# Optimization experiments

Hardware: AMD Instinct MI355X
Metric: run time of the kernel (lower is better)

Reference implementation:

```python
import jax, jax.numpy as jnp
import numpy as np

B, N, D = 8, 1024, 768
R, SH = 10, 2
H = R + SH            # 12 total heads
DH = D // H           # 64
DF = 2 * D            # FFN hidden


def _layernorm(x, g, b, eps=1e-5):
    mu = jnp.mean(x, axis=-1, keepdims=True)
    var = jnp.var(x, axis=-1, keepdims=True)
    return (x - mu) * jax.lax.rsqrt(var + eps) * g + b


def setup_inputs() -> dict:
    key = jax.random.key(0)
    ks = jax.random.split(key, 12)
    s = 0.02
    inp = {
        'nodes': jax.random.normal(ks[0], (B, N, D), dtype=jnp.float32),
        'relation_mask': jax.random.uniform(ks[1], (B, N, N, R), dtype=jnp.float32),
        'node_mask': jax.random.randint(ks[2], (B, N), 0, 2).astype(bool),
        'Wq': jax.random.normal(ks[3], (D, D), dtype=jnp.float32) * s,
        'bq': jnp.zeros((D,), jnp.float32),
        'Wk': jax.random.normal(ks[4], (D, D), dtype=jnp.float32) * s,
        'bk': jnp.zeros((D,), jnp.float32),
        'Wv': jax.random.normal(ks[5], (D, D), dtype=jnp.float32) * s,
        'bv': jnp.zeros((D,), jnp.float32),
        'Wo': jax.random.normal(ks[6], (D, D), dtype=jnp.float32) * s,
        'bo': jnp.zeros((D,), jnp.float32),
        'ln1_g': jnp.ones((D,), jnp.float32),
        'ln1_b': jnp.zeros((D,), jnp.float32),
        'W1': jax.random.normal(ks[7], (DF, D), dtype=jnp.float32) * s,
        'b1': jnp.zeros((DF,), jnp.float32),
        'W2': jax.random.normal(ks[8], (D, DF), dtype=jnp.float32) * s,
        'b2': jnp.zeros((D,), jnp.float32),
        'ln2_g': jnp.ones((D,), jnp.float32),
        'ln2_b': jnp.zeros((D,), jnp.float32),
    }
    return inp


def reference(nodes, relation_mask, node_mask, Wq, bq, Wk, bk, Wv, bv, Wo, bo,
              ln1_g, ln1_b, W1, b1, W2, b2, ln2_g, ln2_b):
    neg_inf = jnp.float32(-jnp.inf)
    # projections -> [B, H, N, DH]
    q = (nodes @ Wq.T + bq).reshape(B, N, H, DH).transpose(0, 2, 1, 3)
    k = (nodes @ Wk.T + bk).reshape(B, N, H, DH).transpose(0, 2, 1, 3)
    v = (nodes @ Wv.T + bv).reshape(B, N, H, DH).transpose(0, 2, 1, 3)
    scores = jnp.einsum('bhqd,bhkd->bhqk', q, k) / jnp.sqrt(jnp.float32(DH))
    # relation-typed gating on first R heads
    rel_gate = relation_mask.transpose(0, 3, 1, 2)          # [B, R, N, N]
    typed = jnp.where(rel_gate < 1e-4, neg_inf, scores[:, :R])
    scores = jnp.concatenate([typed, scores[:, R:]], axis=1)
    # key padding mask
    key_mask = node_mask[:, None, None, :]                  # [B,1,1,N]
    scores = jnp.where(key_mask, scores, neg_inf)
    attn = jax.nn.softmax(scores, axis=-1)
    attn = jnp.nan_to_num(attn, nan=0.0)                    # rows with no valid keys -> 0
    out = jnp.einsum('bhqk,bhkd->bhqd', attn, v)
    out = out.transpose(0, 2, 1, 3).reshape(B, N, D)
    out = out @ Wo.T + bo
    h = _layernorm(nodes + out, ln1_g, ln1_b)
    ffn = jax.nn.gelu(h @ W1.T + b1, approximate=False) @ W2.T + b2
    h = _layernorm(h + ffn, ln2_g, ln2_b)
    return h
```

## Files before the change

### kernel.cpp

```cpp
#include <hip/hip_runtime.h>
#include <stdint.h>
#include <math.h>

typedef unsigned short u16;
typedef __bf16 bf16x8 __attribute__((ext_vector_type(8)));
typedef __bf16 bf16x2 __attribute__((ext_vector_type(2)));
typedef unsigned short u16x8 __attribute__((ext_vector_type(8)));
typedef float f32x4 __attribute__((ext_vector_type(4)));

#define DEVI __device__ __forceinline__

constexpr int B_ = 8, N_ = 1024, D_ = 768, H_ = 12, DH_ = 64, DF_ = 1536;

DEVI u16 f2bu(float f) {
  unsigned x = __builtin_bit_cast(unsigned, f);
  x += 0x7FFFu + ((x >> 16) & 1u);
  return (u16)(x >> 16);
}
DEVI float b2f(u16 u) { return __builtin_bit_cast(float, (unsigned)u << 16); }

DEVI bf16x8 ld_frag(const u16* p) {
  return __builtin_bit_cast(bf16x8, *(const u16x8*)p);
}

DEVI void gload_lds16(const u16* g, u16* l) {
  __builtin_amdgcn_global_load_lds(
      (const __attribute__((address_space(1))) void*)g,
      (__attribute__((address_space(3))) void*)l, 16, 0, 0);
}

struct CvtArgs {
  const float* src[7];
  u16* dst[7];
  int n4[7];
  int start[8];
};
__global__ __launch_bounds__(256)
void prep_all(CvtArgs a, const float* __restrict__ rel, const int* __restrict__ nm,
              u16* __restrict__ mp) {
  const int gb0 = blockIdx.x;
  const int t = threadIdx.x;
  if (gb0 < 2048) {
    const int b = gb0 >> 8, q0 = ((gb0 >> 2) & 63) * 16, k0 = (gb0 & 3) * 256;
    __shared__ u16 w12[16][256];
    const int key_ok = nm[(b << 10) + k0 + t];
    const float th = 1e-4f;
#pragma unroll 1
    for (int it = 0; it < 16; ++it) {
      unsigned bits;
      if (!key_ok) {
        bits = 0xFFFu;
      } else {
        const size_t idx = (((size_t)(b << 10) + q0 + it) << 10) + k0 + t;
        const float2* rp = (const float2*)(rel + idx * 10);
        float2 a0 = rp[0], a1 = rp[1], a2 = rp[2], a3 = rp[3], a4 = rp[4];
        bits  = (a0.x < th ? 1u : 0u)   | (a0.y < th ? 2u : 0u)
              | (a1.x < th ? 4u : 0u)   | (a1.y < th ? 8u : 0u)
              | (a2.x < th ? 16u : 0u)  | (a2.y < th ? 32u : 0u)
              | (a3.x < th ? 64u : 0u)  | (a3.y < th ? 128u : 0u)
              | (a4.x < th ? 256u : 0u) | (a4.y < th ? 512u : 0u);
      }
      w12[it][t ^ ((it & 7) << 1)] = (u16)bits;
    }
    __syncthreads();
    const int ql = t & 15, kt = t >> 4;
    unsigned wv[16];
#pragma unroll
    for (int j2 = 0; j2 < 8; ++j2) {
      const int e = (kt * 16 + j2 * 2) ^ ((ql & 7) << 1);
      wv[j2 * 2] = w12[ql][e];
      wv[j2 * 2 + 1] = w12[ql][e + 1];
    }
#pragma unroll
    for (int h = 0; h < 12; ++h) {
      unsigned word = 0;
#pragma unroll
      for (int j = 0; j < 16; ++j) word |= ((wv[j] >> h) & 1u) << j;
      mp[(((size_t)(b * H_ + h)) * (N_ / 16) + (k0 >> 4) + kt) * N_ + q0 + ql] = (u16)word;
    }
  } else {
    int j = 0;
    while (gb0 >= a.start[j + 1]) ++j;
    const int i = (gb0 - a.start[j]) * 256 + t;
    if (i >= a.n4[j]) return;
    float4 v = ((const float4*)a.src[j])[i];
    ushort4 o;
    o.x = f2bu(v.x); o.y = f2bu(v.y); o.z = f2bu(v.z); o.w = f2bu(v.w);
    ((ushort4*)a.dst[j])[i] = o;
  }
}

template<int EPI>
DEVI void gemm_body(const u16* __restrict__ A, const u16* __restrict__ Bm,
                    const float* __restrict__ bias0, const float* __restrict__ bias1,
                    const float* __restrict__ residf, const u16* __restrict__ residb,
                    u16* __restrict__ out0, u16* __restrict__ out1,
                    int N, int K, int bx, int by,
                    u16 (&As)[3][128 * 32], u16 (&Bs)[3][128 * 32]) {
  const int t = threadIdx.x;
  const int w = t >> 6, l = t & 63;
  const int li = l & 15, grp = l >> 4;
  const int n0 = bx * 128, m0 = by * 128;
  const int wr = w >> 1, wc = w & 1;

  f32x4 acc[4][4] = {};

  const int arow = w * 16 + (l >> 2);
  const int acol = (l & 3) * 8;
  const u16* Ag = A + (size_t)(m0 + arow) * K + acol;
  const u16* Bg = Bm + (size_t)(n0 + arow) * K + acol;
  const int NT = K >> 5;

  auto stage = [&](int buf, int kt) {
    u16* Asw = &As[buf][(w * 16) * 32];
    u16* Bsw = &Bs[buf][(w * 16) * 32];
    const int k0 = kt * 32;
    gload_lds16(Ag + k0, Asw);
    gload_lds16(Ag + (size_t)64 * K + k0, Asw + 64 * 32);
    gload_lds16(Bg + k0, Bsw);
    gload_lds16(Bg + (size_t)64 * K + k0, Bsw + 64 * 32);
  };

  stage(0, 0); stage(1, 1);
  asm volatile("s_waitcnt vmcnt(4)\n\ts_barrier" ::: "memory");

  for (int kt = 0; kt < NT; ++kt) {
    const int bt = kt % 3;
    const bool pre = (kt + 2 < NT);
    if (pre) stage((kt + 2) % 3, kt + 2);
    bf16x8 af[4], bfr[4];
#pragma unroll
    for (int m = 0; m < 4; ++m)
      af[m] = ld_frag(&As[bt][(wr * 64 + m * 16 + li) * 32 + grp * 8]);
#pragma unroll
    for (int n = 0; n < 4; ++n)
      bfr[n] = ld_frag(&Bs[bt][(wc * 64 + n * 16 + li) * 32 + grp * 8]);
    __builtin_amdgcn_s_setprio(1);
#pragma unroll
    for (int m = 0; m < 4; ++m)
#pragma unroll
      for (int n = 0; n < 4; ++n)
        acc[m][n] = __builtin_amdgcn_mfma_f32_16x16x32_bf16(af[m], bfr[n], acc[m][n], 0, 0, 0);
    __builtin_amdgcn_s_setprio(0);
    if (pre) asm volatile("s_waitcnt vmcnt(4) lgkmcnt(0)\n\ts_barrier" ::: "memory");
    else     asm volatile("s_waitcnt vmcnt(0) lgkmcnt(0)\n\ts_barrier" ::: "memory");
  }

#pragma unroll
  for (int m = 0; m < 4; ++m) {
#pragma unroll
    for (int n = 0; n < 4; ++n) {
#pragma unroll
      for (int j = 0; j < 4; ++j) {
        const int row = m0 + wr * 64 + m * 16 + grp * 4 + j;
        const int col = n0 + wc * 64 + n * 16 + li;
        float v = acc[m][n][j];
        if constexpr (EPI == 0) {
          v += (col < D_) ? bias0[col] : bias1[col - D_];
          if (col < D_) v *= 0.125f;
          const int b = row >> 10, i = row & (N_ - 1);
          int c2 = (col < D_) ? col : col - D_;
          u16* dst = (col < D_) ? out0 : out1;
          dst[(((size_t)(b * H_ + (c2 >> 6))) * N_ + i) * DH_ + (c2 & 63)] = f2bu(v);
        } else if constexpr (EPI == 1) {
          v += bias0[row];
          const int b = col >> 10, i = col & (N_ - 1);
          out0[(((size_t)(b * H_ + (row >> 6))) * DH_ + (row & 63)) * N_ + i] = f2bu(v);
        } else if constexpr (EPI == 2) {
          v += bias0[col] + residf[(size_t)row * N + col];
          out0[(size_t)row * N + col] = f2bu(v);
        } else if constexpr (EPI == 3) {
          v += bias0[col];
          float gel = 0.5f * v * (1.0f + erff(v * 0.70710678118654752440f));
          out0[(size_t)row * N + col] = f2bu(gel);
        } else {
          v += bias0[col] + b2f(residb[(size_t)row * N + col]);
          out0[(size_t)row * N + col] = f2bu(v);
        }
      }
    }
  }
}

template<int EPI>
__global__ __launch_bounds__(256, 3)
void gemm_bt(const u16* __restrict__ A, const u16* __restrict__ Bm,
             const float* __restrict__ bias0,
             const float* __restrict__ residf, const u16* __restrict__ residb,
             u16* __restrict__ out0, int N, int K) {
  __shared__ u16 As[3][128 * 32];
  __shared__ u16 Bs[3][128 * 32];
  const int nwg = gridDim.x * gridDim.y;
  int id = blockIdx.y * gridDim.x + blockIdx.x;
  id = (id & 7) * (nwg >> 3) + (id >> 3);
  const int by = id / gridDim.x;
  const int bx = id - by * gridDim.x;
  gemm_body<EPI>(A, Bm, bias0, nullptr, residf, residb, out0, nullptr,
                 N, K, bx, by, As, Bs);
}

__global__ __launch_bounds__(256, 3)
void gemm_qkv(const u16* __restrict__ Xbf, const u16* __restrict__ Wqk,
              const u16* __restrict__ Wv,
              const float* __restrict__ bq, const float* __restrict__ bk,
              const float* __restrict__ bv,
              u16* __restrict__ qb, u16* __restrict__ kb, u16* __restrict__ vTb) {
  __shared__ u16 As[3][128 * 32];
  __shared__ u16 Bs[3][128 * 32];
  constexpr int nwg = 1152;
  int id = blockIdx.x;
  id = (id & 7) * (nwg >> 3) + (id >> 3);
  if (id < 768) {
    const int by = id / 12, bx = id - by * 12;
    gemm_body<0>(Xbf, Wqk, bq, bk, nullptr, nullptr, qb, kb,
                 1536, 768, bx, by, As, Bs);
  } else {
    const int v = id - 768;
    const int by = v / 64, bx = v - by * 64;
    gemm_body<1>(Wv, Xbf, bv, nullptr, nullptr, nullptr, vTb, nullptr,
                 8192, 768, bx, by, As, Bs);
  }
}

__global__ __launch_bounds__(512, 4)
void attn(const u16* __restrict__ q, const u16* __restrict__ k, const u16* __restrict__ vT,
          const u16* __restrict__ mp, u16* __restrict__ outp) {
  const int nwg = gridDim.x;
  const int p = blockIdx.x;
  const int lid = (p & 7) * (nwg >> 3) + (p >> 3);
  const int bh_i = lid >> 3;
  const int qblk = lid & 7;
  const int b = bh_i / H_, h = bh_i - (bh_i / H_) * H_;
  const int w = threadIdx.x >> 6, l = threadIdx.x & 63;
  const int li = l & 15, grp = l >> 4;
  const int qw = qblk * 128 + w * 16;
  const size_t bh = (size_t)bh_i;

  __shared__ u16 Kt[2][64 * 64];
  __shared__ u16 Vt[2][64 * 64];
  __shared__ u16 P[8][16 * 64];

  const u16* kbase = k + bh * N_ * DH_;
  const u16* vbase = vT + bh * DH_ * N_;

  const int srow_off = l >> 3;
  const int sg = l & 7;
  const int r0 = w * 8;
  auto stageK = [&](int buf, int kj0) {
    const int row = r0 + srow_off;
    const int gp = sg ^ (row & 7);
    gload_lds16(kbase + (size_t)(kj0 + row) * DH_ + gp * 8, &Kt[buf][r0 * 64]);
  };
  auto stageV = [&](int buf, int kj0) {
    const int row = r0 + srow_off;
    const int gp = sg ^ (row & 7);
    gload_lds16(vbase + (size_t)row * N_ + kj0 + gp * 8, &Vt[buf][r0 * 64]);
  };

  const u16* qp = q + (bh * N_ + qw) * DH_;
  const bf16x8 bq0 = ld_frag(qp + li * DH_ + grp * 8);
  const bf16x8 bq1 = ld_frag(qp + li * DH_ + 32 + grp * 8);

  f32x4 accO[4] = {};
  float m = -INFINITY, lsum = 0.f;

  u16* Pw = &P[w][0];
  const int sw = (li & 7) << 3;
  const int prow = li * 64;
  const u16* mrow = mp + bh * (N_ / 16) * N_ + qw + li;

  stageK(0, 0); stageV(0, 0);
  __syncthreads();
  int cur = 0;

  for (int kj0 = 0; kj0 < N_; kj0 += 64) {
    if (kj0 + 64 < N_) { stageK(cur ^ 1, kj0 + 64); stageV(cur ^ 1, kj0 + 64); }
    unsigned mword[4];
#pragma unroll
    for (int t = 0; t < 4; ++t) mword[t] = mrow[(size_t)((kj0 >> 4) + t) * N_];

    f32x4 s[4];
    __builtin_amdgcn_s_setprio(1);
#pragma unroll
    for (int t = 0; t < 4; ++t) {
      const int row = t * 16 + li;
      const int rs = row & 7;
      const bf16x8 ka0 = ld_frag(&Kt[cur][row * 64 + ((grp ^ rs) * 8)]);
      const bf16x8 ka1 = ld_frag(&Kt[cur][row * 64 + (((grp + 4) ^ rs) * 8)]);
      f32x4 z = {0.f, 0.f, 0.f, 0.f};
      z = __builtin_amdgcn_mfma_f32_16x16x32_bf16(ka0, bq0, z, 0, 0, 0);
      z = __builtin_amdgcn_mfma_f32_16x16x32_bf16(ka1, bq1, z, 0, 0, 0);
      s[t] = z;
    }
    __builtin_amdgcn_s_setprio(0);

    float sv[16];
#pragma unroll
    for (int t = 0; t < 4; ++t) {
      const unsigned mb = (mword[t] >> (grp * 4)) & 0xFu;
#pragma unroll
      for (int j = 0; j < 4; ++j)
        sv[t * 4 + j] = ((mb >> j) & 1u) ? -INFINITY : s[t][j];
    }
    const float a0 = fmaxf(fmaxf(sv[0], sv[1]), sv[2]);
    const float a1 = fmaxf(fmaxf(sv[3], sv[4]), sv[5]);
    const float a2 = fmaxf(fmaxf(sv[6], sv[7]), sv[8]);
    const float a3 = fmaxf(fmaxf(sv[9], sv[10]), sv[11]);
    const float a4 = fmaxf(fmaxf(sv[12], sv[13]), sv[14]);
    float rmax = fmaxf(fmaxf(fmaxf(a0, a1), fmaxf(a2, a3)), fmaxf(a4, sv[15]));
    rmax = fmaxf(rmax, __shfl_xor(rmax, 16));
    rmax = fmaxf(rmax, __shfl_xor(rmax, 32));
    if (!__all(rmax <= m + 8.f)) {
      const float mnew = fmaxf(m, rmax);
      const float scal = (m == -INFINITY) ? 0.f : __expf(m - mnew);
      lsum *= scal;
#pragma unroll
      for (int t2 = 0; t2 < 4; ++t2) accO[t2] *= scal;
      m = mnew;
    }
    const float msafe = (m == -INFINITY) ? 0.f : m;
    float psum = 0.f;
    float pv[16];
#pragma unroll
    for (int i = 0; i < 16; ++i) {
      const float e = __expf(sv[i] - msafe);
      pv[i] = e;
      psum += e;
    }
    psum += __shfl_xor(psum, 16);
    psum += __shfl_xor(psum, 32);
    lsum += psum;
#pragma unroll
    for (int t = 0; t < 4; ++t) {
      bf16x2 plo = { (__bf16)pv[t * 4 + 0], (__bf16)pv[t * 4 + 1] };
      bf16x2 phi = { (__bf16)pv[t * 4 + 2], (__bf16)pv[t * 4 + 3] };
      uint2 pk;
      pk.x = __builtin_bit_cast(unsigned, plo);
      pk.y = __builtin_bit_cast(unsigned, phi);
      *(uint2*)&Pw[prow + ((t * 16 + grp * 4) ^ sw)] = pk;
    }
    __builtin_amdgcn_s_setprio(1);
#pragma unroll
    for (int kc = 0; kc < 2; ++kc) {
      const bf16x8 pb = ld_frag(&Pw[prow + ((kc * 32 + grp * 8) ^ sw)]);
#pragma unroll
      for (int t2 = 0; t2 < 4; ++t2) {
        const int row = t2 * 16 + li;
        const bf16x8 va = ld_frag(&Vt[cur][row * 64 + (((kc * 4 + grp) ^ (row & 7)) * 8)]);
        accO[t2] = __builtin_amdgcn_mfma_f32_16x16x32_bf16(va, pb, accO[t2], 0, 0, 0);
      }
    }
    __builtin_amdgcn_s_setprio(0);
    __syncthreads();
    cur ^= 1;
  }
  const float inv = (lsum > 0.f) ? 1.0f / lsum : 0.f;
  u16* op = outp + ((size_t)b * N_ + qw + li) * D_ + h * DH_;
#pragma unroll
  for (int t2 = 0; t2 < 4; ++t2) {
    bf16x2 o01 = { (__bf16)(accO[t2][0] * inv), (__bf16)(accO[t2][1] * inv) };
    bf16x2 o23 = { (__bf16)(accO[t2][2] * inv), (__bf16)(accO[t2][3] * inv) };
    uint2 ov;
    ov.x = __builtin_bit_cast(unsigned, o01);
    ov.y = __builtin_bit_cast(unsigned, o23);
    *(uint2*)&op[t2 * 16 + grp * 4] = ov;
  }
}

template<int OUTF32>
__global__ __launch_bounds__(256)
void ln_kernel(const u16* __restrict__ x, const float* __restrict__ g,
               const float* __restrict__ be, u16* __restrict__ ybf,
               float* __restrict__ yf) {
  const int row = blockIdx.x;
  const int t = threadIdx.x;
  const u16* xr = x + (size_t)row * D_;
  const float v0 = b2f(xr[t]), v1 = b2f(xr[t + 256]), v2 = b2f(xr[t + 512]);
  float s = v0 + v1 + v2;
  float s2 = v0 * v0 + v1 * v1 + v2 * v2;
#pragma unroll
  for (int d = 1; d < 64; d <<= 1) { s += __shfl_xor(s, d); s2 += __shfl_xor(s2, d); }
  __shared__ float red[8];
  const int w = t >> 6;
  if ((t & 63) == 0) { red[w] = s; red[4 + w] = s2; }
  __syncthreads();
  s = red[0] + red[1] + red[2] + red[3];
  s2 = red[4] + red[5] + red[6] + red[7];
  const float mu = s * (1.0f / D_);
  const float var = fmaxf(s2 * (1.0f / D_) - mu * mu, 0.0f);
  const float rstd = rsqrtf(var + 1e-5f);
#pragma unroll
  for (int c = 0; c < 3; ++c) {
    const int idx = t + c * 256;
    const float vv = (c == 0) ? v0 : (c == 1) ? v1 : v2;
    const float o = (vv - mu) * rstd * g[idx] + be[idx];
    if constexpr (OUTF32) yf[(size_t)row * D_ + idx] = o;
    else ybf[(size_t)row * D_ + idx] = f2bu(o);
  }
}

extern "C" void kernel_launch(void* const* d_in, const int* in_sizes, int n_in,
                              void* d_out, int out_size, void* d_ws, size_t ws_size,
                              hipStream_t stream) {
  (void)in_sizes; (void)n_in; (void)out_size; (void)ws_size;
  const float* nodes = (const float*)d_in[0];
  const float* rel   = (const float*)d_in[1];
  const int*   nmask = (const int*)d_in[2];
  const float* Wq = (const float*)d_in[3];
  const float* bq = (const float*)d_in[4];
  const float* Wk = (const float*)d_in[5];
  const float* bk = (const float*)d_in[6];
  const float* Wv = (const float*)d_in[7];
  const float* bv = (const float*)d_in[8];
  const float* Wo = (const float*)d_in[9];
  const float* bo = (const float*)d_in[10];
  const float* ln1g = (const float*)d_in[11];
  const float* ln1b = (const float*)d_in[12];
  const float* W1 = (const float*)d_in[13];
  const float* b1 = (const float*)d_in[14];
  const float* W2 = (const float*)d_in[15];
  const float* b2 = (const float*)d_in[16];
  const float* ln2g = (const float*)d_in[17];
  const float* ln2b = (const float*)d_in[18];
  float* out = (float*)d_out;

  char* ws = (char*)d_ws;
  u16* Wqk_bf = (u16*)(ws + 0);
  u16* Wv_bf  = (u16*)(ws + 2359296);
  u16* Wo_bf  = (u16*)(ws + 3538944);
  u16* W1_bf  = (u16*)(ws + 4718592);
  u16* W2_bf  = (u16*)(ws + 7077888);
  u16* Xbf    = (u16*)(ws + 9437184);
  u16* qb     = (u16*)(ws + 22020096);
  u16* kb     = (u16*)(ws + 34603008);
  u16* vTb    = (u16*)(ws + 47185920);
  u16* mwb    = (u16*)(ws + 59768832);
  u16* prehb  = (u16*)(ws + 22020096);
  u16* hbf    = (u16*)(ws + 47185920);
  u16* f1b    = (u16*)(ws + 59768832);
  u16* preob  = (u16*)(ws + 84934656);
  u16* attno  = Xbf;

  const dim3 blk(256);
  CvtArgs ca;
  ca.src[0] = Wq; ca.src[1] = Wk; ca.src[2] = Wv; ca.src[3] = Wo;
  ca.src[4] = W1; ca.src[5] = W2; ca.src[6] = nodes;
  ca.dst[0] = Wqk_bf; ca.dst[1] = Wqk_bf + 768 * 768; ca.dst[2] = Wv_bf;
  ca.dst[3] = Wo_bf; ca.dst[4] = W1_bf; ca.dst[5] = W2_bf; ca.dst[6] = Xbf;
  ca.n4[0] = ca.n4[1] = ca.n4[2] = ca.n4[3] = 147456;
  ca.n4[4] = ca.n4[5] = 294912; ca.n4[6] = 1572864;
  ca.start[0] = 2048; ca.start[1] = 2624; ca.start[2] = 3200; ca.start[3] = 3776;
  ca.start[4] = 4352; ca.start[5] = 5504; ca.start[6] = 6656; ca.start[7] = 12800;
  prep_all<<<12800, blk, 0, stream>>>(ca, rel, nmask, mwb);
  gemm_qkv<<<1152, blk, 0, stream>>>(Xbf, Wqk_bf, Wv_bf, bq, bk, bv, qb, kb, vTb);
  attn<<<768, dim3(512), 0, stream>>>(qb, kb, vTb, mwb, attno);
  gemm_bt<2><<<dim3(6, 64), blk, 0, stream>>>(attno, Wo_bf, bo, nodes, nullptr,
                                              prehb, 768, 768);
  ln_kernel<0><<<8192, blk, 0, stream>>>(prehb, ln1g, ln1b, hbf, nullptr);
  gemm_bt<3><<<dim3(12, 64), blk, 0, stream>>>(hbf, W1_bf, b1, nullptr, nullptr,
                                               f1b, 1536, 768);
  gemm_bt<4><<<dim3(6, 64), blk, 0, stream>>>(f1b, W2_bf, b2, nullptr, hbf,
                                              preob, 768, 1536);
  ln_kernel<1><<<8192, blk, 0, stream>>>(preob, ln2g, ln2b, nullptr, out);
}
```

Baseline: 298.5 us.

## Fuse relation-mask packing into QKV GEMM kernel to overlap bandwidth and compute

The relation-mask bit-packing work, which streams the large fp32 relation tensor, moves out of the conversion kernel and into the QKV GEMM launch. Blocks are interleaved in groups of 16 mask blocks and 9 GEMM tiles, so the memory-bound mask work runs alongside the matrix-core GEMM. The mask blocks reuse the GEMM's LDS buffer as scratch. The cost is that mask blocks now carry the GEMM kernel's LDS allocation and launch bounds, which can lower their occupancy, and the tile swizzle is recomputed.

Result: slower. 312.0 us (+4.5%).

```diff
diff --git a/kernel.cpp b/kernel.cpp
--- a/kernel.cpp
+++ b/kernel.cpp
@@ -36,58 +36,16 @@
   int start[8];
 };
 __global__ __launch_bounds__(256)
-void prep_all(CvtArgs a, const float* __restrict__ rel, const int* __restrict__ nm,
-              u16* __restrict__ mp) {
-  const int gb0 = blockIdx.x;
-  const int t = threadIdx.x;
-  if (gb0 < 2048) {
-    const int b = gb0 >> 8, q0 = ((gb0 >> 2) & 63) * 16, k0 = (gb0 & 3) * 256;
-    __shared__ u16 w12[16][256];
-    const int key_ok = nm[(b << 10) + k0 + t];
-    const float th = 1e-4f;
-#pragma unroll 1
-    for (int it = 0; it < 16; ++it) {
-      unsigned bits;
-      if (!key_ok) {
-        bits = 0xFFFu;
-      } else {
-        const size_t idx = (((size_t)(b << 10) + q0 + it) << 10) + k0 + t;
-        const float2* rp = (const float2*)(rel + idx * 10);
-        float2 a0 = rp[0], a1 = rp[1], a2 = rp[2], a3 = rp[3], a4 = rp[4];
-        bits  = (a0.x < th ? 1u : 0u)   | (a0.y < th ? 2u : 0u)
-              | (a1.x < th ? 4u : 0u)   | (a1.y < th ? 8u : 0u)
-              | (a2.x < th ? 16u : 0u)  | (a2.y < th ? 32u : 0u)
-              | (a3.x < th ? 64u : 0u)  | (a3.y < th ? 128u : 0u)
-              | (a4.x < th ? 256u : 0u) | (a4.y < th ? 512u : 0u);
-      }
-      w12[it][t ^ ((it & 7) << 1)] = (u16)bits;
-    }
-    __syncthreads();
-    const int ql = t & 15, kt = t >> 4;
-    unsigned wv[16];
-#pragma unroll
-    for (int j2 = 0; j2 < 8; ++j2) {
-      const int e = (kt * 16 + j2 * 2) ^ ((ql & 7) << 1);
-      wv[j2 * 2] = w12[ql][e];
-      wv[j2 * 2 + 1] = w12[ql][e + 1];
-    }
-#pragma unroll
-    for (int h = 0; h < 12; ++h) {
-      unsigned word = 0;
-#pragma unroll
-      for (int j = 0; j < 16; ++j) word |= ((wv[j] >> h) & 1u) << j;
-      mp[(((size_t)(b * H_ + h)) * (N_ / 16) + (k0 >> 4) + kt) * N_ + q0 + ql] = (u16)word;
-    }
-  } else {
-    int j = 0;
-    while (gb0 >= a.start[j + 1]) ++j;
-    const int i = (gb0 - a.start[j]) * 256 + t;
-    if (i >= a.n4[j]) return;
-    float4 v = ((const float4*)a.src[j])[i];
-    ushort4 o;
-    o.x = f2bu(v.x); o.y = f2bu(v.y); o.z = f2bu(v.z); o.w = f2bu(v.w);
-    ((ushort4*)a.dst[j])[i] = o;
-  }
+void cvt_all(CvtArgs a) {
+  const int gb = blockIdx.x;
+  int j = 0;
+  while (gb >= a.start[j + 1]) ++j;
+  const int i = (gb - a.start[j]) * 256 + threadIdx.x;
+  if (i >= a.n4[j]) return;
+  float4 v = ((const float4*)a.src[j])[i];
+  ushort4 o;
+  o.x = f2bu(v.x); o.y = f2bu(v.y); o.z = f2bu(v.z); o.w = f2bu(v.w);
+  ((ushort4*)a.dst[j])[i] = o;
 }
 
 template<int EPI>
@@ -200,25 +158,70 @@
 }
 
 __global__ __launch_bounds__(256, 3)
-void gemm_qkv(const u16* __restrict__ Xbf, const u16* __restrict__ Wqk,
+void mask_qkv(const float* __restrict__ rel, const int* __restrict__ nm,
+              u16* __restrict__ mp,
+              const u16* __restrict__ Xbf, const u16* __restrict__ Wqk,
               const u16* __restrict__ Wv,
               const float* __restrict__ bq, const float* __restrict__ bk,
               const float* __restrict__ bv,
               u16* __restrict__ qb, u16* __restrict__ kb, u16* __restrict__ vTb) {
   __shared__ u16 As[3][128 * 32];
   __shared__ u16 Bs[3][128 * 32];
-  constexpr int nwg = 1152;
-  int id = blockIdx.x;
-  id = (id & 7) * (nwg >> 3) + (id >> 3);
-  if (id < 768) {
-    const int by = id / 12, bx = id - by * 12;
-    gemm_body<0>(Xbf, Wqk, bq, bk, nullptr, nullptr, qb, kb,
-                 1536, 768, bx, by, As, Bs);
+  const int id0 = blockIdx.x;
+  const int g = id0 / 25, r = id0 - g * 25;
+  const int t = threadIdx.x;
+  if (r < 16) {
+    const int mb = g * 16 + r;
+    const int b = mb >> 8, q0 = ((mb >> 2) & 63) * 16, k0 = (mb & 3) * 256;
+    u16 (*w12)[256] = (u16(*)[256])&As[0][0];
+    const int key_ok = nm[(b << 10) + k0 + t];
+    const float th = 1e-4f;
+#pragma unroll 1
+    for (int it = 0; it < 16; ++it) {
+      unsigned bits;
+      if (!key_ok) {
+        bits = 0xFFFu;
+      } else {
+        const size_t idx = (((size_t)(b << 10) + q0 + it) << 10) + k0 + t;
+        const float2* rp = (const float2*)(rel + idx * 10);
+        float2 a0 = rp[0], a1 = rp[1], a2 = rp[2], a3 = rp[3], a4 = rp[4];
+        bits  = (a0.x < th ? 1u : 0u)   | (a0.y < th ? 2u : 0u)
+              | (a1.x < th ? 4u : 0u)   | (a1.y < th ? 8u : 0u)
+              | (a2.x < th ? 16u : 0u)  | (a2.y < th ? 32u : 0u)
+              | (a3.x < th ? 64u : 0u)  | (a3.y < th ? 128u : 0u)
+              | (a4.x < th ? 256u : 0u) | (a4.y < th ? 512u : 0u);
+      }
+      w12[it][t ^ ((it & 7) << 1)] = (u16)bits;
+    }
+    __syncthreads();
+    const int ql = t & 15, kt = t >> 4;
+    unsigned wv[16];
+#pragma unroll
+    for (int j2 = 0; j2 < 8; ++j2) {
+      const int e = (kt * 16 + j2 * 2) ^ ((ql & 7) << 1);
+      wv[j2 * 2] = w12[ql][e];
+      wv[j2 * 2 + 1] = w12[ql][e + 1];
+    }
+#pragma unroll
+    for (int h = 0; h < 12; ++h) {
+      unsigned word = 0;
+#pragma unroll
+      for (int j = 0; j < 16; ++j) word |= ((wv[j] >> h) & 1u) << j;
+      mp[(((size_t)(b * H_ + h)) * (N_ / 16) + (k0 >> 4) + kt) * N_ + q0 + ql] = (u16)word;
+    }
   } else {
-    const int v = id - 768;
-    const int by = v / 64, bx = v - by * 64;
-    gemm_body<1>(Wv, Xbf, bv, nullptr, nullptr, nullptr, vTb, nullptr,
-                 8192, 768, bx, by, As, Bs);
+    int gid = g * 9 + (r - 16);
+    gid = (gid & 7) * 144 + (gid >> 3);
+    if (gid < 768) {
+      const int by = gid / 12, bx = gid - by * 12;
+      gemm_body<0>(Xbf, Wqk, bq, bk, nullptr, nullptr, qb, kb,
+                   1536, 768, bx, by, As, Bs);
+    } else {
+      const int v = gid - 768;
+      const int by = v / 64, bx = v - by * 64;
+      gemm_body<1>(Wv, Xbf, bv, nullptr, nullptr, nullptr, vTb, nullptr,
+                   8192, 768, bx, by, As, Bs);
+    }
   }
 }
 
@@ -449,10 +452,11 @@
   ca.dst[3] = Wo_bf; ca.dst[4] = W1_bf; ca.dst[5] = W2_bf; ca.dst[6] = Xbf;
   ca.n4[0] = ca.n4[1] = ca.n4[2] = ca.n4[3] = 147456;
   ca.n4[4] = ca.n4[5] = 294912; ca.n4[6] = 1572864;
-  ca.start[0] = 2048; ca.start[1] = 2624; ca.start[2] = 3200; ca.start[3] = 3776;
-  ca.start[4] = 4352; ca.start[5] = 5504; ca.start[6] = 6656; ca.start[7] = 12800;
-  prep_all<<<12800, blk, 0, stream>>>(ca, rel, nmask, mwb);
-  gemm_qkv<<<1152, blk, 0, stream>>>(Xbf, Wqk_bf, Wv_bf, bq, bk, bv, qb, kb, vTb);
+  ca.start[0] = 0; ca.start[1] = 576; ca.start[2] = 1152; ca.start[3] = 1728;
+  ca.start[4] = 2304; ca.start[5] = 3456; ca.start[6] = 4608; ca.start[7] = 10752;
+  cvt_all<<<10752, blk, 0, stream>>>(ca);
+  mask_qkv<<<3200, blk, 0, stream>>>(rel, nmask, mwb, Xbf, Wqk_bf, Wv_bf,
+                                     bq, bk, bv, qb, kb, vTb);
   attn<<<768, dim3(512), 0, stream>>>(qb, kb, vTb, mwb, attno);
   gemm_bt<2><<<dim3(6, 64), blk, 0, stream>>>(attno, Wo_bf, bo, nodes, nullptr,
                                               prehb, 768, 768);
```

## Compact valid keys per batch and skip masked keys in mask, V, and attention

Applied to the files above, without the earlier changes.

A new compaction kernel builds, per batch, a list of valid key indices and a padded count. Mask building, the V projection and the attention loop then run only over those compacted keys, skipping padded-out keys; K is gathered through the index list and V^T is written in compacted order. Separately, the Q scale absorbs log2(e) so the softmax uses exp2f with an adjusted rescale threshold. This adds an extra launch and gather indirection, and the speedup depends on the fraction of masked keys (about half with random masks).

After: 312.3 us. +4.6%, slower.

```diff
diff --git a/kernel.cpp b/kernel.cpp
--- a/kernel.cpp
+++ b/kernel.cpp
@@ -11,6 +11,8 @@
 #define DEVI __device__ __forceinline__
 
 constexpr int B_ = 8, N_ = 1024, D_ = 768, H_ = 12, DH_ = 64, DF_ = 1536;
+constexpr float QSCALE = 0.18033688011112042f;
+constexpr float THR2 = 11.5415603f;
 
 DEVI u16 f2bu(float f) {
   unsigned x = __builtin_bit_cast(unsigned, f);
@@ -27,6 +29,28 @@
   __builtin_amdgcn_global_load_lds(
       (const __attribute__((address_space(1))) void*)g,
       (__attribute__((address_space(3))) void*)l, 16, 0, 0);
+}
+
+__global__ __launch_bounds__(1024)
+void compact(const int* __restrict__ nm, int* __restrict__ idx,
+             int* __restrict__ nkparr) {
+  const int b = blockIdx.x, t = threadIdx.x;
+  const int wave = t >> 6, lane = t & 63;
+  const bool valid = nm[b * N_ + t] != 0;
+  const unsigned long long ball = __ballot(valid);
+  const int pre = (int)__popcll(ball & ((1ull << lane) - 1ull));
+  __shared__ int wsum[16];
+  if (lane == 0) wsum[wave] = (int)__popcll(ball);
+  __syncthreads();
+  int base = 0;
+#pragma unroll
+  for (int i = 0; i < 16; ++i) base += (i < wave) ? wsum[i] : 0;
+  int total = 0;
+#pragma unroll
+  for (int i = 0; i < 16; ++i) total += wsum[i];
+  if (valid) idx[b * N_ + base + pre] = t;
+  if (t < N_ - total) idx[b * N_ + total + t] = 0;
+  if (t == 0) { nkparr[b] = (total + 63) & ~63; nkparr[8 + b] = total; }
 }
 
 struct CvtArgs {
@@ -36,23 +60,28 @@
   int start[8];
 };
 __global__ __launch_bounds__(256)
-void prep_all(CvtArgs a, const float* __restrict__ rel, const int* __restrict__ nm,
+void prep_all(CvtArgs a, const float* __restrict__ rel,
+              const int* __restrict__ idx, const int* __restrict__ nkparr,
               u16* __restrict__ mp) {
   const int gb0 = blockIdx.x;
   const int t = threadIdx.x;
   if (gb0 < 2048) {
     const int b = gb0 >> 8, q0 = ((gb0 >> 2) & 63) * 16, k0 = (gb0 & 3) * 256;
+    const int nkp = nkparr[b], nk = nkparr[8 + b];
+    if (k0 >= nkp) return;
+    const int s = k0 + t;
+    const int tok = idx[b * N_ + s];
+    const bool vs = (s < nk);
     __shared__ u16 w12[16][256];
-    const int key_ok = nm[(b << 10) + k0 + t];
     const float th = 1e-4f;
 #pragma unroll 1
     for (int it = 0; it < 16; ++it) {
       unsigned bits;
-      if (!key_ok) {
+      if (!vs) {
         bits = 0xFFFu;
       } else {
-        const size_t idx = (((size_t)(b << 10) + q0 + it) << 10) + k0 + t;
-        const float2* rp = (const float2*)(rel + idx * 10);
+        const size_t ridx = (((size_t)(b << 10) + q0 + it) << 10) + tok;
+        const float2* rp = (const float2*)(rel + ridx * 10);
         float2 a0 = rp[0], a1 = rp[1], a2 = rp[2], a3 = rp[3], a4 = rp[4];
         bits  = (a0.x < th ? 1u : 0u)   | (a0.y < th ? 2u : 0u)
               | (a1.x < th ? 4u : 0u)   | (a1.y < th ? 8u : 0u)
@@ -157,15 +186,11 @@
         float v = acc[m][n][j];
         if constexpr (EPI == 0) {
           v += (col < D_) ? bias0[col] : bias1[col - D_];
-          if (col < D_) v *= 0.125f;
+          if (col < D_) v *= QSCALE;
           const int b = row >> 10, i = row & (N_ - 1);
           int c2 = (col < D_) ? col : col - D_;
           u16* dst = (col < D_) ? out0 : out1;
           dst[(((size_t)(b * H_ + (c2 >> 6))) * N_ + i) * DH_ + (c2 & 63)] = f2bu(v);
-        } else if constexpr (EPI == 1) {
-          v += bias0[row];
-          const int b = col >> 10, i = col & (N_ - 1);
-          out0[(((size_t)(b * H_ + (row >> 6))) * DH_ + (row & 63)) * N_ + i] = f2bu(v);
         } else if constexpr (EPI == 2) {
           v += bias0[col] + residf[(size_t)row * N + col];
           out0[(size_t)row * N + col] = f2bu(v);
@@ -177,6 +202,77 @@
           v += bias0[col] + b2f(residb[(size_t)row * N + col]);
           out0[(size_t)row * N + col] = f2bu(v);
         }
+      }
+    }
+  }
+}
+
+DEVI void gemm_v_body(const u16* __restrict__ Wv, const u16* __restrict__ Xbf,
+                      const float* __restrict__ bv, const int* __restrict__ idxb,
+                      int b, int tile, int c, u16* __restrict__ vTb,
+                      u16 (&As)[3][128 * 32], u16 (&Bs)[3][128 * 32]) {
+  constexpr int K = 768, NT = 24;
+  const int t = threadIdx.x;
+  const int w = t >> 6, l = t & 63;
+  const int li = l & 15, grp = l >> 4;
+  const int wr = w >> 1, wc = w & 1;
+  const int m0 = c * 128;
+
+  f32x4 acc[4][4] = {};
+
+  const int arow = w * 16 + (l >> 2);
+  const int acol = (l & 3) * 8;
+  const int tok0 = idxb[tile * 128 + arow];
+  const int tok1 = idxb[tile * 128 + arow + 64];
+  const u16* Ag = Wv + (size_t)(m0 + arow) * K + acol;
+  const u16* Bg0 = Xbf + ((size_t)b * N_ + tok0) * K + acol;
+  const u16* Bg1 = Xbf + ((size_t)b * N_ + tok1) * K + acol;
+
+  auto stage = [&](int buf, int kt) {
+    u16* Asw = &As[buf][(w * 16) * 32];
+    u16* Bsw = &Bs[buf][(w * 16) * 32];
+    const int k0 = kt * 32;
+    gload_lds16(Ag + k0, Asw);
+    gload_lds16(Ag + (size_t)64 * K + k0, Asw + 64 * 32);
+    gload_lds16(Bg0 + k0, Bsw);
+    gload_lds16(Bg1 + k0, Bsw + 64 * 32);
+  };
+
+  stage(0, 0); stage(1, 1);
+  asm volatile("s_waitcnt vmcnt(4)\n\ts_barrier" ::: "memory");
+
+  for (int kt = 0; kt < NT; ++kt) {
+    const int bt = kt % 3;
+    const bool pre = (kt + 2 < NT);
+    if (pre) stage((kt + 2) % 3, kt + 2);
+    bf16x8 af[4], bfr[4];
+#pragma unroll
+    for (int m = 0; m < 4; ++m)
+      af[m] = ld_frag(&As[bt][(wr * 64 + m * 16 + li) * 32 + grp * 8]);
+#pragma unroll
+    for (int n = 0; n < 4; ++n)
+      bfr[n] = ld_frag(&Bs[bt][(wc * 64 + n * 16 + li) * 32 + grp * 8]);
+    __builtin_amdgcn_s_setprio(1);
+#pragma unroll
+    for (int m = 0; m < 4; ++m)
+#pragma unroll
+      for (int n = 0; n < 4; ++n)
+        acc[m][n] = __builtin_amdgcn_mfma_f32_16x16x32_bf16(af[m], bfr[n], acc[m][n], 0, 0, 0);
+    __builtin_amdgcn_s_setprio(0);
+    if (pre) asm volatile("s_waitcnt vmcnt(4) lgkmcnt(0)\n\ts_barrier" ::: "memory");
+    else     asm volatile("s_waitcnt vmcnt(0) lgkmcnt(0)\n\ts_barrier" ::: "memory");
+  }
+
+  u16* outb = vTb + (size_t)b * D_ * N_;
+#pragma unroll
+  for (int m = 0; m < 4; ++m) {
+#pragma unroll
+    for (int n = 0; n < 4; ++n) {
+      const int slot = tile * 128 + wc * 64 + n * 16 + li;
+#pragma unroll
+      for (int j = 0; j < 4; ++j) {
+        const int row = m0 + wr * 64 + m * 16 + grp * 4 + j;
+        outb[(size_t)row * N_ + slot] = f2bu(acc[m][n][j] + bv[row]);
       }
     }
   }
@@ -204,6 +300,7 @@
               const u16* __restrict__ Wv,
               const float* __restrict__ bq, const float* __restrict__ bk,
               const float* __restrict__ bv,
+              const int* __restrict__ idx, const int* __restrict__ nkparr,
               u16* __restrict__ qb, u16* __restrict__ kb, u16* __restrict__ vTb) {
   __shared__ u16 As[3][128 * 32];
   __shared__ u16 Bs[3][128 * 32];
@@ -215,16 +312,18 @@
     gemm_body<0>(Xbf, Wqk, bq, bk, nullptr, nullptr, qb, kb,
                  1536, 768, bx, by, As, Bs);
   } else {
-    const int v = id - 768;
-    const int by = v / 64, bx = v - by * 64;
-    gemm_body<1>(Wv, Xbf, bv, nullptr, nullptr, nullptr, vTb, nullptr,
-                 8192, 768, bx, by, As, Bs);
+    const int vs = id - 768;
+    const int c = vs / 64, ts = vs - c * 64;
+    const int b = ts >> 3, tile = ts & 7;
+    if (tile * 128 >= nkparr[b]) return;
+    gemm_v_body(Wv, Xbf, bv, idx + b * N_, b, tile, c, vTb, As, Bs);
   }
 }
 
 __global__ __launch_bounds__(512, 4)
 void attn(const u16* __restrict__ q, const u16* __restrict__ k, const u16* __restrict__ vT,
-          const u16* __restrict__ mp, u16* __restrict__ outp) {
+          const u16* __restrict__ mp, const int* __restrict__ idx,
+          const int* __restrict__ nkparr, u16* __restrict__ outp) {
   const int nwg = gridDim.x;
   const int p = blockIdx.x;
   const int lid = (p & 7) * (nwg >> 3) + (p >> 3);
@@ -235,6 +334,8 @@
   const int li = l & 15, grp = l >> 4;
   const int qw = qblk * 128 + w * 16;
   const size_t bh = (size_t)bh_i;
+  const int nkp = nkparr[b];
+  const int* idxb = idx + b * N_;
 
   __shared__ u16 Kt[2][64 * 64];
   __shared__ u16 Vt[2][64 * 64];
@@ -248,8 +349,9 @@
   const int r0 = w * 8;
   auto stageK = [&](int buf, int kj0) {
     const int row = r0 + srow_off;
+    const int tok = idxb[kj0 + row];
     const int gp = sg ^ (row & 7);
-    gload_lds16(kbase + (size_t)(kj0 + row) * DH_ + gp * 8, &Kt[buf][r0 * 64]);
+    gload_lds16(kbase + (size_t)tok * DH_ + gp * 8, &Kt[buf][r0 * 64]);
   };
   auto stageV = [&](int buf, int kj0) {
     const int row = r0 + srow_off;
@@ -269,12 +371,12 @@
   const int prow = li * 64;
   const u16* mrow = mp + bh * (N_ / 16) * N_ + qw + li;
 
-  stageK(0, 0); stageV(0, 0);
+  if (nkp > 0) { stageK(0, 0); stageV(0, 0); }
   __syncthreads();
   int cur = 0;
 
-  for (int kj0 = 0; kj0 < N_; kj0 += 64) {
-    if (kj0 + 64 < N_) { stageK(cur ^ 1, kj0 + 64); stageV(cur ^ 1, kj0 + 64); }
+  for (int kj0 = 0; kj0 < nkp; kj0 += 64) {
+    if (kj0 + 64 < nkp) { stageK(cur ^ 1, kj0 + 64); stageV(cur ^ 1, kj0 + 64); }
     unsigned mword[4];
 #pragma unroll
     for (int t = 0; t < 4; ++t) mword[t] = mrow[(size_t)((kj0 >> 4) + t) * N_];
@@ -310,9 +412,9 @@
     float rmax = fmaxf(fmaxf(fmaxf(a0, a1), fmaxf(a2, a3)), fmaxf(a4, sv[15]));
     rmax = fmaxf(rmax, __shfl_xor(rmax, 16));
     rmax = fmaxf(rmax, __shfl_xor(rmax, 32));
-    if (!__all(rmax <= m + 8.f)) {
+    if (!__all(rmax <= m + THR2)) {
       const float mnew = fmaxf(m, rmax);
-      const float scal = (m == -INFINITY) ? 0.f : __expf(m - mnew);
+      const float scal = (m == -INFINITY) ? 0.f : exp2f(m - mnew);
       lsum *= scal;
 #pragma unroll
       for (int t2 = 0; t2 < 4; ++t2) accO[t2] *= scal;
@@ -323,7 +425,7 @@
     float pv[16];
 #pragma unroll
     for (int i = 0; i < 16; ++i) {
-      const float e = __expf(sv[i] - msafe);
+      const float e = exp2f(sv[i] - msafe);
       pv[i] = e;
       psum += e;
     }
@@ -391,11 +493,11 @@
   const float rstd = rsqrtf(var + 1e-5f);
 #pragma unroll
   for (int c = 0; c < 3; ++c) {
-    const int idx = t + c * 256;
+    const int idx2 = t + c * 256;
     const float vv = (c == 0) ? v0 : (c == 1) ? v1 : v2;
-    const float o = (vv - mu) * rstd * g[idx] + be[idx];
-    if constexpr (OUTF32) yf[(size_t)row * D_ + idx] = o;
-    else ybf[(size_t)row * D_ + idx] = f2bu(o);
+    const float o = (vv - mu) * rstd * g[idx2] + be[idx2];
+    if constexpr (OUTF32) yf[(size_t)row * D_ + idx2] = o;
+    else ybf[(size_t)row * D_ + idx2] = f2bu(o);
   }
 }
 
@@ -439,9 +541,12 @@
   u16* hbf    = (u16*)(ws + 47185920);
   u16* f1b    = (u16*)(ws + 59768832);
   u16* preob  = (u16*)(ws + 84934656);
+  int* idx    = (int*)(ws + 100663296);
+  int* nkparr = (int*)(ws + 100696064);
   u16* attno  = Xbf;
 
   const dim3 blk(256);
+  compact<<<8, dim3(1024), 0, stream>>>(nmask, idx, nkparr);
   CvtArgs ca;
   ca.src[0] = Wq; ca.src[1] = Wk; ca.src[2] = Wv; ca.src[3] = Wo;
   ca.src[4] = W1; ca.src[5] = W2; ca.src[6] = nodes;
@@ -451,9 +556,10 @@
   ca.n4[4] = ca.n4[5] = 294912; ca.n4[6] = 1572864;
   ca.start[0] = 2048; ca.start[1] = 2624; ca.start[2] = 3200; ca.start[3] = 3776;
   ca.start[4] = 4352; ca.start[5] = 5504; ca.start[6] = 6656; ca.start[7] = 12800;
-  prep_all<<<12800, blk, 0, stream>>>(ca, rel, nmask, mwb);
-  gemm_qkv<<<1152, blk, 0, stream>>>(Xbf, Wqk_bf, Wv_bf, bq, bk, bv, qb, kb, vTb);
-  attn<<<768, dim3(512), 0, stream>>>(qb, kb, vTb, mwb, attno);
+  prep_all<<<12800, blk, 0, stream>>>(ca, rel, idx, nkparr, mwb);
+  gemm_qkv<<<1152, blk, 0, stream>>>(Xbf, Wqk_bf, Wv_bf, bq, bk, bv,
+                                     idx, nkparr, qb, kb, vTb);
+  attn<<<768, dim3(512), 0, stream>>>(qb, kb, vTb, mwb, idx, nkparr, attno);
   gemm_bt<2><<<dim3(6, 64), blk, 0, stream>>>(attno, Wo_bf, bo, nodes, nullptr,
                                               prehb, 768, 768);
   ln_kernel<0><<<8192, blk, 0, stream>>>(prehb, ln1g, ln1b, hbf, nullptr);
```
